# Optimization experiments

Measured on AMD Instinct MI355X. Metric: run time of the kernel, lower is better.

## Reference

```python
import jax, jax.numpy as jnp
import numpy as np

B, P2, TOPK, W2, C_KV = 4, 64, 16, 49, 512


def setup_inputs() -> dict:
    key = jax.random.key(0)
    k1, k2 = jax.random.split(key)
    r_idx = jax.random.randint(k1, (B, P2, TOPK), 0, P2, dtype=jnp.int64)
    kv = jax.random.normal(k2, (B, P2, W2, C_KV), dtype=jnp.float32)
    return {"r_idx": r_idx, "kv": kv}


def reference(r_idx, kv):
    # kv: (b, p2, w2, c_kv); r_idx: (b, p2, topk) with values in [0, p2)
    # Output: (b, p2, topk, w2, c_kv) -- gather top-k regions per query region.
    # Direct advanced indexing avoids materializing the (b, p2, p2, w2, c_kv)
    # expanded tensor the torch version broadcasts before gathering.
    b = kv.shape[0]
    batch_idx = jnp.arange(b)[:, None, None]  # (b, 1, 1) broadcasts against (b, p2, topk)
    topk_kv = kv[batch_idx, r_idx]            # (b, p2, topk, w2, c_kv)
    return topk_kv
```

## Files before the change

### kernel.cpp

```cpp
#include <hip/hip_runtime.h>


constexpr int B    = 4;
constexpr int P2   = 64;
constexpr int TOPK = 16;
constexpr int W2   = 49;
constexpr int C_KV = 512;
constexpr int REGION = W2 * C_KV;
constexpr int REGION4 = REGION / 4;
constexpr int NBLOCKS = B * P2 * TOPK;
constexpr int TPB = 256;

typedef float floatx4 __attribute__((ext_vector_type(4)));

__global__ __launch_bounds__(TPB) void kvgather_kernel(
    const int* __restrict__ r_idx,
    const float* __restrict__ kv,
    float* __restrict__ out)
{
    const int bpt = blockIdx.x;
    const int b   = bpt >> 10;
    const int src = r_idx[bpt];

    const floatx4* __restrict__ s =
        (const floatx4*)(kv + ((size_t)(b * P2 + src)) * REGION);
    floatx4* __restrict__ d =
        (floatx4*)(out + (size_t)bpt * REGION);

    for (int i = threadIdx.x; i < REGION4; i += TPB) {
        floatx4 v = s[i];
        __builtin_nontemporal_store(v, &d[i]);
    }
}

extern "C" void kernel_launch(void* const* d_in, const int* in_sizes, int n_in,
                              void* d_out, int out_size, void* d_ws, size_t ws_size,
                              hipStream_t stream) {
    const int*   r_idx = (const int*)d_in[0];
    const float* kv    = (const float*)d_in[1];
    float*       out   = (float*)d_out;

    kvgather_kernel<<<NBLOCKS, TPB, 0, stream>>>(r_idx, kv, out);
}
```

Before: 460.1 us.

## Invert gather to source-major scatter so each kv region is read once

Result: faster. 433.2 us (-5.9%).

```diff
diff --git a/kernel.cpp b/kernel.cpp
--- a/kernel.cpp
+++ b/kernel.cpp
@@ -6,30 +6,58 @@
 constexpr int TOPK = 16;
 constexpr int W2   = 49;
 constexpr int C_KV = 512;
-constexpr int REGION = W2 * C_KV;
+constexpr int REGION  = W2 * C_KV;
 constexpr int REGION4 = REGION / 4;
-constexpr int NBLOCKS = B * P2 * TOPK;
-constexpr int TPB = 256;
+constexpr int PT      = P2 * TOPK;
+constexpr int CHUNKS  = 8;
+constexpr int CHUNK4  = REGION4 / CHUNKS;
+constexpr int TPB     = 256;
+constexpr int NBLOCKS = B * P2 * CHUNKS;
 
 typedef float floatx4 __attribute__((ext_vector_type(4)));
 
-__global__ __launch_bounds__(TPB) void kvgather_kernel(
+__global__ __launch_bounds__(TPB) void kvgather_srcmajor(
     const int* __restrict__ r_idx,
     const float* __restrict__ kv,
     float* __restrict__ out)
 {
-    const int bpt = blockIdx.x;
-    const int b   = bpt >> 10;
-    const int src = r_idx[bpt];
+    const int blk = blockIdx.x;
+    const int c   = blk & (CHUNKS - 1);
+    const int bs  = blk >> 3;
+    const int b   = bs >> 6;
+    const int src = bs & (P2 - 1);
 
-    const floatx4* __restrict__ s =
-        (const floatx4*)(kv + ((size_t)(b * P2 + src)) * REGION);
-    floatx4* __restrict__ d =
-        (floatx4*)(out + (size_t)bpt * REGION);
+    __shared__ int s_cnt;
+    __shared__ int s_base4[PT];
 
-    for (int i = threadIdx.x; i < REGION4; i += TPB) {
-        floatx4 v = s[i];
-        __builtin_nontemporal_store(v, &d[i]);
+    if (threadIdx.x == 0) s_cnt = 0;
+    __syncthreads();
+
+    {
+        const int4 rv = ((const int4*)(r_idx + b * PT))[threadIdx.x];
+        const int vals[4] = { rv.x, rv.y, rv.z, rv.w };
+        #pragma unroll
+        for (int j = 0; j < 4; ++j) {
+            if (vals[j] == src) {
+                const int pos = atomicAdd(&s_cnt, 1);
+                s_base4[pos] = (b * PT + threadIdx.x * 4 + j) * REGION4;
+            }
+        }
+    }
+    __syncthreads();
+    const int n = s_cnt;
+    if (n == 0) return;
+
+    const floatx4* __restrict__ s4 = (const floatx4*)kv + (size_t)bs * REGION4;
+    floatx4* __restrict__ o4 = (floatx4*)out;
+
+    const int i0 = c * CHUNK4;
+    const int i1 = i0 + CHUNK4;
+    for (int i = i0 + threadIdx.x; i < i1; i += TPB) {
+        const floatx4 v = s4[i];
+        for (int k = 0; k < n; ++k) {
+            __builtin_nontemporal_store(v, o4 + (size_t)(s_base4[k] + i));
+        }
     }
 }
 
@@ -40,5 +68,5 @@
     const float* kv    = (const float*)d_in[1];
     float*       out   = (float*)d_out;
 
-    kvgather_kernel<<<NBLOCKS, TPB, 0, stream>>>(r_idx, kv, out);
+    kvgather_srcmajor<<<NBLOCKS, TPB, 0, stream>>>(r_idx, kv, out);
 }
```
